# Performance work log

Hardware: AMD Instinct MI355X
Metric: run time of the kernel (lower is better)

## Reference

```python
import jax, jax.numpy as jnp
import numpy as np

B, IN, ED, PW, OUT, CL, NK = 2048, 4096, 8192, 2048, 256, 16, 32
MIX = 0.5

def _onehot_mask(key, n):
    # near-one-hot selector matrix [n, NK], as built by forward_update_masks
    idx = jax.random.choice(key, n, (NK,), replace=False)
    return jnp.zeros((n, NK), jnp.float32).at[idx, jnp.arange(NK)].set(1.0)

def setup_inputs():
    ks = jax.random.split(jax.random.key(0), 24)
    f = jnp.float32
    adj = (jax.random.uniform(ks[4], (IN, IN)) < 0.01).astype(f)
    adj = jnp.maximum(adj, adj.T).at[jnp.arange(IN), jnp.arange(IN)].set(1.0)
    return {
        'x_gene': jax.random.normal(ks[0], (B, IN), f),
        'x_invmea': jax.random.normal(ks[1], (B, IN), f),
        'x_curv': jax.random.normal(ks[2], (B, ED), f),
        'clinn': jax.random.normal(ks[3], (B, CL), f),
        'Adj': adj,
        'edge_mask': (jax.random.uniform(ks[5], (ED, IN)) < 0.005).astype(f),
        'pathway_mask': (jax.random.uniform(ks[6], (PW, ED)) < 0.02).astype(f),
        'top_gene_mask': _onehot_mask(ks[7], IN),
        'top_invmea_mask': _onehot_mask(ks[8], IN),
        'top_curv_mask': _onehot_mask(ks[9], ED),
        'top_path_mask': _onehot_mask(ks[10], PW),
        'W1': jnp.full((IN, IN), 0.05, f),
        'b1': 0.01 * jax.random.normal(ks[11], (IN,), f),
        'W2': jnp.full((ED, IN), 0.05, f),
        'b2': 0.01 * jax.random.normal(ks[12], (ED,), f),
        'W3': jnp.full((PW, ED), 0.05, f),
        'b3': 0.01 * jax.random.normal(ks[13], (PW,), f),
        'W4': 0.02 * jax.random.normal(ks[14], (OUT, PW), f),
        'b4': 0.01 * jax.random.normal(ks[15], (OUT,), f),
        'W5': 0.02 * jax.random.normal(ks[16], (OUT, OUT), f),
        'b5': 0.01 * jax.random.normal(ks[17], (OUT,), f),
        'W6': 0.05 * jax.random.normal(ks[18], (OUT, OUT + CL + 4 * NK), f),
        'W7': 0.05 * jax.random.normal(ks[19], (1, OUT), f),
        'mp11': MIX * jnp.ones(IN, f),
        'mp12': (1.0 - MIX) * jnp.ones(IN, f),
        'mp1': jnp.ones(IN, f),
        'mp21': MIX * jnp.ones(ED, f),
        'mp22': (1.0 - MIX) * jnp.ones(ED, f),
        'mp2': jnp.ones(ED, f),
        'mp3': jnp.ones(PW, f),
    }

def reference(x_gene, x_invmea, x_curv, clinn, Adj, edge_mask, pathway_mask,
              top_gene_mask, top_invmea_mask, top_curv_mask, top_path_mask,
              W1, b1, W2, b2, W3, b3, W4, b4, W5, b5, W6, W7,
              mp11, mp12, mp1, mp21, mp22, mp2, mp3):
    sg = jax.lax.stop_gradient
    sig = jax.nn.sigmoid
    kept_gene = sg(x_gene @ top_gene_mask)                     # [B,NK] gather-as-matmul
    x1 = sig(x_gene @ (W1 * Adj).T + b1)                       # masked linear [B,IN]
    x1 = x_invmea * (mp11 * mp1) + x1 * (mp12 * mp1)
    kept_invmea = sg(x1 @ top_invmea_mask)
    x1 = sig(x1 @ (W2 * edge_mask).T + b2)                     # [B,ED]
    x1 = x_curv * (mp21 * mp2) + x1 * (mp22 * mp2)
    kept_curv = sg(x1 @ top_curv_mask)
    x1 = sig(x1 @ (W3 * pathway_mask).T + b3)                  # [B,PW]
    x1 = x1 * mp3
    kept_path = sg(x1 @ top_path_mask)
    x1 = sig(x1 @ W4.T + b4)
    x1 = sig(x1 @ W5.T + b5)                                   # [B,OUT]
    x_cat = jnp.concatenate([x1, kept_gene, kept_invmea, kept_curv, kept_path, clinn], axis=1)
    lp = sig(x_cat @ W6.T)
    lp = lp - jnp.mean(lp, axis=1, keepdims=True)
    return lp @ W7.T                                           # [B,1]
```

## Files before the change

### kernel.cpp

```cpp
#include <hip/hip_runtime.h>

typedef unsigned short u16;
typedef __attribute__((ext_vector_type(4))) float f32x4;
typedef __attribute__((ext_vector_type(8))) short s16x8;

__device__ __forceinline__ u16 f2bf(float f) {
    union { float f; unsigned u; } c; c.f = f;
    return (u16)((c.u + 0x7fffu + ((c.u >> 16) & 1u)) >> 16);
}
__device__ __forceinline__ float bf2f(u16 u) {
    union { unsigned u; float f; } c; c.u = ((unsigned)u) << 16; return c.f;
}
__device__ __forceinline__ unsigned pk2(float a, float b) {
    return (unsigned)f2bf(a) | ((unsigned)f2bf(b) << 16);
}
__device__ __forceinline__ float sigm(float x) { return 1.0f / (1.0f + __expf(-x)); }
__device__ __forceinline__ void fma2(unsigned xv, float w, float& a0, float& a1) {
    union { float f; unsigned u; } lo, hi;
    lo.u = xv << 16; hi.u = xv & 0xFFFF0000u;
    a0 += w * lo.f; a1 += w * hi.f;
}

__device__ __forceinline__ void load16_g2l(const void* g, void* l) {
    __builtin_amdgcn_global_load_lds(
        (const __attribute__((address_space(1))) unsigned int*)(unsigned long long)g,
        (__attribute__((address_space(3))) unsigned int*)(unsigned int)(unsigned long long)l,
        16, 0, 0);
}

__device__ void d_transpF(const float* __restrict__ in, u16* __restrict__ out,
                          int Rr, int Cc, int bx, int by, float (*t)[65]) {
    const int r0 = by * 64, c0 = bx * 64;
    const int tid = threadIdx.x;
#pragma unroll
    for (int i = 0; i < 16; i++) {
        int idx = tid + i * 256;
        int rr = idx >> 6, cc = idx & 63;
        t[rr][cc] = in[(size_t)(r0 + rr) * Cc + c0 + cc];
    }
    __syncthreads();
#pragma unroll
    for (int i = 0; i < 16; i++) {
        int idx = tid + i * 256;
        int cc = idx >> 6, rr = idx & 63;
        out[(size_t)(c0 + cc) * Rr + r0 + rr] = f2bf(t[rr][cc]);
    }
}

__device__ void d_ell(const float* __restrict__ M, const float* __restrict__ W,
                      unsigned* __restrict__ ell, int* __restrict__ cnt,
                      int C, int PAD, int R, int bid) {
    const int lane = threadIdx.x & 63;
    const int row = bid * 4 + (threadIdx.x >> 6);
    if (row >= R) return;
    const float* mrow = M + (size_t)row * C;
    const float* wrow = W + (size_t)row * C;
    int n = 0;
    for (int c = lane * 4; c < C; c += 256) {
        float4 m = *(const float4*)(mrow + c);
        n += (m.x != 0.f) + (m.y != 0.f) + (m.z != 0.f) + (m.w != 0.f);
    }
    int pre = n;
#pragma unroll
    for (int off = 1; off < 64; off <<= 1) {
        int t = __shfl_up(pre, off, 64);
        if (lane >= off) pre += t;
    }
    int s = pre - n;
    unsigned* erow = ell + (size_t)row * PAD;
    for (int c = lane * 4; c < C; c += 256) {
        float4 m = *(const float4*)(mrow + c);
        if (m.x != 0.f) { if (s < PAD) erow[s] = ((unsigned)f2bf(wrow[c + 0]) << 16) | (unsigned)(c + 0); s++; }
        if (m.y != 0.f) { if (s < PAD) erow[s] = ((unsigned)f2bf(wrow[c + 1]) << 16) | (unsigned)(c + 1); s++; }
        if (m.z != 0.f) { if (s < PAD) erow[s] = ((unsigned)f2bf(wrow[c + 2]) << 16) | (unsigned)(c + 2); s++; }
        if (m.w != 0.f) { if (s < PAD) erow[s] = ((unsigned)f2bf(wrow[c + 3]) << 16) | (unsigned)(c + 3); s++; }
    }
    int tot = __shfl(pre, 63, 64);
    if (lane == 0) cnt[row] = tot > PAD ? PAD : tot;
}

__device__ void d_find(const float* __restrict__ mask, int n, int* __restrict__ outp,
                       int* red) {
    int best = -1;
    for (int i = threadIdx.x; i < n; i += 256)
        if (mask[(size_t)i * 32 + (blockIdx.x & 31)] != 0.0f) best = i;
    red[threadIdx.x] = best;
    __syncthreads();
    for (int off = 128; off > 0; off >>= 1) {
        if (threadIdx.x < off) {
            int o = red[threadIdx.x + off];
            if (o > red[threadIdx.x]) red[threadIdx.x] = o;
        }
        __syncthreads();
    }
    if (threadIdx.x == 0) *outp = red[0] < 0 ? 0 : red[0];
}

__device__ void d_conv(const float* __restrict__ in, u16* __restrict__ out,
                       int bid, unsigned n8) {
    unsigned i = bid * 256u + threadIdx.x;
    if (i >= n8) return;
    float4 a = ((const float4*)in)[2 * i];
    float4 b = ((const float4*)in)[2 * i + 1];
    uint4 o;
    o.x = pk2(a.x, a.y); o.y = pk2(a.z, a.w);
    o.z = pk2(b.x, b.y); o.w = pk2(b.z, b.w);
    ((uint4*)out)[i] = o;
}

__global__ __launch_bounds__(256) void prep_all(
    const float* __restrict__ xg_f, const float* __restrict__ xinv_f,
    const float* __restrict__ xcv_f,
    u16* __restrict__ xTg, u16* __restrict__ xinvT, u16* __restrict__ xcvT,
    const float* __restrict__ Adj, const float* __restrict__ W1,
    unsigned* __restrict__ ell1, int* __restrict__ cnt1,
    const float* __restrict__ edge, const float* __restrict__ W2,
    unsigned* __restrict__ ell2, int* __restrict__ cnt2,
    const float* __restrict__ path, const float* __restrict__ W3,
    unsigned* __restrict__ ell3, int* __restrict__ cnt3,
    const float* __restrict__ m0, const float* __restrict__ m1,
    const float* __restrict__ m2, const float* __restrict__ m3,
    int* __restrict__ idx,
    const float* __restrict__ W4, u16* __restrict__ w4b,
    const float* __restrict__ W5, u16* __restrict__ w5b) {
    __shared__ float tile[64][65];
    int id = blockIdx.x;
    if (id < 2048) { d_transpF(xg_f, xTg, 2048, 4096, id & 63, id >> 6, tile); return; }
    id -= 2048;
    if (id < 2048) { d_transpF(xinv_f, xinvT, 2048, 4096, id & 63, id >> 6, tile); return; }
    id -= 2048;
    if (id < 4096) { d_transpF(xcv_f, xcvT, 2048, 8192, id & 127, id >> 7, tile); return; }
    id -= 4096;
    if (id < 1024) { d_ell(Adj, W1, ell1, cnt1, 4096, 256, 4096, id); return; }
    id -= 1024;
    if (id < 2048) { d_ell(edge, W2, ell2, cnt2, 4096, 96, 8192, id); return; }
    id -= 2048;
    if (id < 512) { d_ell(path, W3, ell3, cnt3, 8192, 320, 2048, id); return; }
    id -= 512;
    if (id < 128) {
        const float* mk; int n;
        int which = id >> 5;
        if (which == 0)      { mk = m0; n = 4096; }
        else if (which == 1) { mk = m1; n = 4096; }
        else if (which == 2) { mk = m2; n = 8192; }
        else                 { mk = m3; n = 2048; }
        d_find(mk, n, idx + which * 32 + (id & 31), (int*)tile);
        return;
    }
    id -= 128;
    if (id < 256) { d_conv(W4, w4b, id, 65536u); return; }
    id -= 256;
    d_conv(W5, w5b, id, 8192u);
}

template <int BPL>
__global__ __launch_bounds__(256) void spmm(const unsigned* __restrict__ ell,
                                            const int* __restrict__ cnt,
                                            const u16* __restrict__ xT,
                                            u16* __restrict__ outT,
                                            const float* __restrict__ bias,
                                            const float* __restrict__ c1a,
                                            const float* __restrict__ c1b,
                                            const float* __restrict__ c2a,
                                            const float* __restrict__ c2b,
                                            const u16* __restrict__ invT,
                                            int PAD) {
    const int lane = threadIdx.x & 63;
    const int wv = __builtin_amdgcn_readfirstlane((int)(threadIdx.x >> 6));
    const int j = blockIdx.y * 4 + wv;
    const int b0 = blockIdx.x * (64 * BPL) + lane * BPL;

    const unsigned* ep = ell + (size_t)j * PAD;
    int len = cnt[j];
    if (len > PAD) len = PAD;

    float acc[BPL];
#pragma unroll
    for (int i = 0; i < BPL; i++) acc[i] = 0.f;

    const int nfull = len >> 3;
    unsigned eA[8];
    if (nfull > 0) {
#pragma unroll
        for (int t = 0; t < 8; t++) eA[t] = ep[t];
    }
    for (int g = 0; g < nfull; g++) {
        unsigned eB[8];
        const bool more = (g + 1 < nfull);
        if (more) {
#pragma unroll
            for (int t = 0; t < 8; t++) eB[t] = ep[(g + 1) * 8 + t];
        }
        if (BPL == 8) {
            uint4 xv[8];
#pragma unroll
            for (int t = 0; t < 8; t++)
                xv[t] = *(const uint4*)(xT + ((size_t)(eA[t] & 0xFFFFu) << 11) + b0);
#pragma unroll
            for (int t = 0; t < 8; t++) {
                union { float f; unsigned u; } w; w.u = (eA[t] >> 16) << 16;
                fma2(xv[t].x, w.f, acc[0], acc[1]);
                fma2(xv[t].y, w.f, acc[2], acc[3]);
                fma2(xv[t].z, w.f, acc[4], acc[5]);
                fma2(xv[t].w, w.f, acc[6], acc[7]);
            }
        } else {
            uint2 xv[8];
#pragma unroll
            for (int t = 0; t < 8; t++)
                xv[t] = *(const uint2*)(xT + ((size_t)(eA[t] & 0xFFFFu) << 11) + b0);
#pragma unroll
            for (int t = 0; t < 8; t++) {
                union { float f; unsigned u; } w; w.u = (eA[t] >> 16) << 16;
                fma2(xv[t].x, w.f, acc[0], acc[1]);
                fma2(xv[t].y, w.f, acc[2], acc[3]);
            }
        }
        if (more) {
#pragma unroll
            for (int t = 0; t < 8; t++) eA[t] = eB[t];
        }
    }
    for (int s = nfull * 8; s < len; ++s) {
        unsigned e = ep[s];
        union { float f; unsigned u; } w; w.u = (e >> 16) << 16;
        const u16* xp = xT + ((size_t)(e & 0xFFFFu) << 11) + b0;
        if (BPL == 8) {
            uint4 xv = *(const uint4*)xp;
            fma2(xv.x, w.f, acc[0], acc[1]); fma2(xv.y, w.f, acc[2], acc[3]);
            fma2(xv.z, w.f, acc[4], acc[5]); fma2(xv.w, w.f, acc[6], acc[7]);
        } else {
            uint2 xv = *(const uint2*)xp;
            fma2(xv.x, w.f, acc[0], acc[1]); fma2(xv.y, w.f, acc[2], acc[3]);
        }
    }

    const float bi = bias[j];
    float c1 = 0.f;
    if (c1a) { c1 = c1a[j]; if (c1b) c1 *= c1b[j]; }
    float c2 = 1.f;
    if (c2a) { c2 = c2a[j]; if (c2b) c2 *= c2b[j]; }

    float v[BPL];
#pragma unroll
    for (int i = 0; i < BPL; i++) v[i] = sigm(acc[i] + bi) * c2;
    if (invT) {
        const unsigned long long* ip = (const unsigned long long*)(invT + ((size_t)j << 11) + b0);
#pragma unroll
        for (int h = 0; h < BPL / 4; h++) {
            unsigned long long iv = __builtin_nontemporal_load(ip + h);
            unsigned lo = (unsigned)iv, hi = (unsigned)(iv >> 32);
            union { float f; unsigned u; } g0, g1, g2, g3;
            g0.u = lo << 16; g1.u = lo & 0xFFFF0000u;
            g2.u = hi << 16; g3.u = hi & 0xFFFF0000u;
            v[4 * h + 0] += g0.f * c1; v[4 * h + 1] += g1.f * c1;
            v[4 * h + 2] += g2.f * c1; v[4 * h + 3] += g3.f * c1;
        }
    }
    unsigned long long* op = (unsigned long long*)(outT + ((size_t)j << 11) + b0);
#pragma unroll
    for (int h = 0; h < BPL / 4; h++) {
        unsigned long long ov = (unsigned long long)pk2(v[4 * h + 0], v[4 * h + 1])
                              | ((unsigned long long)pk2(v[4 * h + 2], v[4 * h + 3]) << 32);
        __builtin_nontemporal_store(ov, op + h);
    }
}

__global__ __launch_bounds__(256) void gatherFT(const float* __restrict__ src, int ld,
                                                const int* __restrict__ idx,
                                                u16* __restrict__ dstT) {
    int i = blockIdx.x * 256 + threadIdx.x;
    int kk = i >> 11, b = i & 2047;
    dstT[i] = f2bf(src[(size_t)b * ld + idx[kk]]);
}
__global__ __launch_bounds__(256) void gatherT(const u16* __restrict__ xT,
                                               const int* __restrict__ idx,
                                               u16* __restrict__ dstT) {
    int i = blockIdx.x * 256 + threadIdx.x;
    int kk = i >> 11, b = i & 2047;
    dstT[i] = xT[(size_t)idx[kk] * 2048 + b];
}

__global__ __launch_bounds__(256) void transpB(const u16* __restrict__ in,
                                               u16* __restrict__ out, int Rr, int Cc) {
    __shared__ u16 t[64][66];
    const int r0 = blockIdx.y * 64, c0 = blockIdx.x * 64;
    const int tid = threadIdx.x;
#pragma unroll
    for (int i = 0; i < 16; i++) {
        int idx = tid + i * 256;
        int rr = idx >> 6, cc = idx & 63;
        t[rr][cc] = in[(size_t)(r0 + rr) * Cc + c0 + cc];
    }
    __syncthreads();
#pragma unroll
    for (int i = 0; i < 16; i++) {
        int idx = tid + i * 256;
        int cc = idx >> 6, rr = idx & 63;
        out[(size_t)(c0 + cc) * Rr + r0 + rr] = t[rr][cc];
    }
}

template <int WR, int WC, int MF, int NF, int KC, int WPE>
__global__ __launch_bounds__(WR * WC * 64, WPE)
void gemm_t(const u16* __restrict__ A, const u16* __restrict__ W,
            u16* __restrict__ Out, const float* __restrict__ bias, int N, int K) {
    constexpr int NTHR = WR * WC * 64;
    constexpr int BM = WR * MF * 16;
    constexpr int BN = WC * NF * 16;
    constexpr int BK = KC * 32;
    constexpr int CPR = KC * 4;
    constexpr int MSK = CPR - 1;
    constexpr int CA = BM * CPR / NTHR;
    constexpr int CB = BN * CPR / NTHR;
    constexpr int L  = CA + CB;

    __shared__ u16 At[2][BM * BK];
    __shared__ u16 Bt[2][BN * BK];

    const int tid = threadIdx.x;
    const int lane = tid & 63;
    const int wave = tid >> 6;
    const int wr = wave / WC, wc = wave % WC;
    const int tn = blockIdx.x, tm = blockIdx.y;
    const int r16 = lane & 15;
    const int q = lane >> 4;

    const u16* aSrc[CA]; int aDst[CA];
#pragma unroll
    for (int j = 0; j < CA; j++) {
        int c = tid + j * NTHR;
        int r = c / CPR, p = c - r * CPR;
        aSrc[j] = A + (size_t)(tm * BM + r) * K + (p ^ (r & MSK)) * 8;
        aDst[j] = c * 8;
    }
    const u16* bSrc[CB]; int bDst[CB];
#pragma unroll
    for (int j = 0; j < CB; j++) {
        int c = tid + j * NTHR;
        int r = c / CPR, p = c - r * CPR;
        bSrc[j] = W + (size_t)(tn * BN + r) * K + (p ^ (r & MSK)) * 8;
        bDst[j] = c * 8;
    }
    int aRd[MF][KC], bRd[NF][KC];
#pragma unroll
    for (int mi = 0; mi < MF; mi++)
#pragma unroll
        for (int kc = 0; kc < KC; kc++)
            aRd[mi][kc] = (wr * MF * 16 + mi * 16 + r16) * BK + (((kc * 4 + q) ^ (r16 & MSK)) << 3);
#pragma unroll
    for (int ni = 0; ni < NF; ni++)
#pragma unroll
        for (int kc = 0; kc < KC; kc++)
            bRd[ni][kc] = (wc * NF * 16 + ni * 16 + r16) * BK + (((kc * 4 + q) ^ (r16 & MSK)) << 3);

    const int nIter = K / BK;

#define ISSUE(slot, it_)                                              \
    do {                                                              \
        const int k0_ = (it_) * BK;                                   \
        _Pragma("unroll")                                             \
        for (int j = 0; j < CA; j++)                                  \
            load16_g2l(aSrc[j] + k0_, &At[slot][aDst[j]]);            \
        _Pragma("unroll")                                             \
        for (int j = 0; j < CB; j++)                                  \
            load16_g2l(bSrc[j] + k0_, &Bt[slot][bDst[j]]);            \
    } while (0)

    ISSUE(0, 0);
    if (nIter > 1) ISSUE(1, 1);

    f32x4 acc[MF][NF];
#pragma unroll
    for (int i = 0; i < MF; i++)
#pragma unroll
        for (int j = 0; j < NF; j++) acc[i][j] = (f32x4){0.f, 0.f, 0.f, 0.f};

    for (int it = 0; it < nIter; ++it) {
        const int s = it & 1;
        if (it + 1 < nIter) __builtin_amdgcn_s_waitcnt(0xF70 | L);
        else                __builtin_amdgcn_s_waitcnt(0xF70);
        __asm__ volatile("" ::: "memory");
        __builtin_amdgcn_s_barrier();
        __asm__ volatile("" ::: "memory");

        s16x8 af[KC][MF], bfr[KC][NF];
#pragma unroll
        for (int kc = 0; kc < KC; kc++) {
#pragma unroll
            for (int mi = 0; mi < MF; mi++) af[kc][mi] = *(const s16x8*)(&At[s][aRd[mi][kc]]);
#pragma unroll
            for (int ni = 0; ni < NF; ni++) bfr[kc][ni] = *(const s16x8*)(&Bt[s][bRd[ni][kc]]);
        }
        __asm__ volatile("" ::: "memory");
        __builtin_amdgcn_s_waitcnt(0xC07F);
        __builtin_amdgcn_s_barrier();
        __asm__ volatile("" ::: "memory");

        if (it + 2 < nIter) ISSUE(s, it + 2);

#pragma unroll
        for (int kc = 0; kc < KC; kc++)
#pragma unroll
            for (int mi = 0; mi < MF; mi++)
#pragma unroll
                for (int ni = 0; ni < NF; ni++)
                    acc[mi][ni] = __builtin_amdgcn_mfma_f32_16x16x32_bf16(af[kc][mi], bfr[kc][ni], acc[mi][ni], 0, 0, 0);
    }
#undef ISSUE

#pragma unroll
    for (int ni = 0; ni < NF; ni++) {
        const int n = tn * BN + wc * NF * 16 + ni * 16 + r16;
        const float bi = bias ? bias[n] : 0.f;
#pragma unroll
        for (int mi = 0; mi < MF; mi++) {
#pragma unroll
            for (int rg = 0; rg < 4; rg++) {
                const int m = tm * BM + wr * MF * 16 + mi * 16 + q * 4 + rg;
                Out[(size_t)m * N + n] = f2bf(sigm(acc[mi][ni][rg] + bi));
            }
        }
    }
}

__global__ __launch_bounds__(256) void tail_k(const u16* __restrict__ x5,
                                              const u16* __restrict__ kgT,
                                              const u16* __restrict__ kiT,
                                              const u16* __restrict__ kcT,
                                              const u16* __restrict__ kpT,
                                              const float* __restrict__ clinn,
                                              const float* __restrict__ W6,
                                              const float* __restrict__ W7,
                                              float* __restrict__ out) {
    __shared__ float xs[8 * 400];
    __shared__ float s1[4][8], s2[4][8], s3[4];
    const int tid = threadIdx.x;
    const int b0 = blockIdx.x * 8;
    for (int i = tid; i < 8 * 400; i += 256) {
        int r = i / 400, c = i - r * 400;
        int b = b0 + r;
        float v;
        if (c < 256)      v = bf2f(x5[b * 256 + c]);
        else if (c < 288) v = bf2f(kgT[(c - 256) * 2048 + b]);
        else if (c < 320) v = bf2f(kiT[(c - 288) * 2048 + b]);
        else if (c < 352) v = bf2f(kcT[(c - 320) * 2048 + b]);
        else if (c < 384) v = bf2f(kpT[(c - 352) * 2048 + b]);
        else              v = clinn[b * 16 + (c - 384)];
        xs[i] = v;
    }
    __syncthreads();
    const int j = tid;
    float acc[8];
#pragma unroll
    for (int r = 0; r < 8; r++) acc[r] = 0.f;
    const float4* wrow = (const float4*)(W6 + (size_t)j * 400);
    for (int c = 0; c < 100; c++) {
        float4 wv = wrow[c];
        const float* wp = (const float*)&wv;
#pragma unroll
        for (int t = 0; t < 4; t++) {
            float w = wp[t];
            int k = c * 4 + t;
#pragma unroll
            for (int r = 0; r < 8; r++) acc[r] += w * xs[r * 400 + k];
        }
    }
    const float w7j = W7[j];
    const int lane = tid & 63, wave = tid >> 6;
    float t3 = w7j;
#pragma unroll
    for (int off = 32; off > 0; off >>= 1) t3 += __shfl_down(t3, off, 64);
    if (lane == 0) s3[wave] = t3;
#pragma unroll
    for (int r = 0; r < 8; r++) {
        float lp = sigm(acc[r]);
        float t1 = lp, t2 = lp * w7j;
#pragma unroll
        for (int off = 32; off > 0; off >>= 1) {
            t1 += __shfl_down(t1, off, 64);
            t2 += __shfl_down(t2, off, 64);
        }
        if (lane == 0) { s1[wave][r] = t1; s2[wave][r] = t2; }
    }
    __syncthreads();
    if (tid < 8) {
        float S1 = s1[0][tid] + s1[1][tid] + s1[2][tid] + s1[3][tid];
        float S2 = s2[0][tid] + s2[1][tid] + s2[2][tid] + s2[3][tid];
        float SW = s3[0] + s3[1] + s3[2] + s3[3];
        out[b0 + tid] = S2 - (S1 * (1.f / 256.f)) * SW;
    }
}

extern "C" void kernel_launch(void* const* d_in, const int* in_sizes, int n_in,
                              void* d_out, int out_size, void* d_ws, size_t ws_size,
                              hipStream_t stream) {
    const float* x_gene   = (const float*)d_in[0];
    const float* x_invmea = (const float*)d_in[1];
    const float* x_curv   = (const float*)d_in[2];
    const float* clinn    = (const float*)d_in[3];
    const float* Adj      = (const float*)d_in[4];
    const float* edge_m   = (const float*)d_in[5];
    const float* path_m   = (const float*)d_in[6];
    const float* tg_mask  = (const float*)d_in[7];
    const float* ti_mask  = (const float*)d_in[8];
    const float* tc_mask  = (const float*)d_in[9];
    const float* tp_mask  = (const float*)d_in[10];
    const float* W1 = (const float*)d_in[11];  const float* b1 = (const float*)d_in[12];
    const float* W2 = (const float*)d_in[13];  const float* b2 = (const float*)d_in[14];
    const float* W3 = (const float*)d_in[15];  const float* b3 = (const float*)d_in[16];
    const float* W4 = (const float*)d_in[17];  const float* b4 = (const float*)d_in[18];
    const float* W5 = (const float*)d_in[19];  const float* b5 = (const float*)d_in[20];
    const float* W6 = (const float*)d_in[21];
    const float* W7 = (const float*)d_in[22];
    const float* mp11 = (const float*)d_in[23];
    const float* mp12 = (const float*)d_in[24];
    const float* mp1  = (const float*)d_in[25];
    const float* mp21 = (const float*)d_in[26];
    const float* mp22 = (const float*)d_in[27];
    const float* mp2  = (const float*)d_in[28];
    const float* mp3  = (const float*)d_in[29];

    char* ws = (char*)d_ws;
    const float* nulf = nullptr;
    float* out = (float*)d_out;

    u16*  xTg   = (u16*)(ws + 0);
    u16*  xinvT = (u16*)(ws + 16777216);
    u16*  xcvT  = (u16*)(ws + 33554432);
    u16*  x1T   = (u16*)(ws + 67108864);
    u16*  x2T   = (u16*)(ws + 83886080);
    u16*  x3T   = (u16*)(ws + 117440512);
    u16*  x3    = (u16*)(ws + 125829120);
    unsigned* ell1 = (unsigned*)(ws + 134217728);
    unsigned* ell2 = (unsigned*)(ws + 138412032);
    unsigned* ell3 = (unsigned*)(ws + 141557760);
    int* cnt1 = (int*)(ws + 144179200);
    int* cnt2 = (int*)(ws + 144195584);
    int* cnt3 = (int*)(ws + 144228352);
    int* idxg = (int*)(ws + 144236544);
    int* idxi = idxg + 32;
    int* idxc = idxg + 64;
    int* idxp = idxg + 96;
    u16* kgT  = (u16*)(ws + 144237056);
    u16* kiT  = (u16*)(ws + 144368128);
    u16* kcT  = (u16*)(ws + 144499200);
    u16* kpT  = (u16*)(ws + 144630272);
    u16* w4b  = (u16*)(ws + 144761344);
    u16* w5b  = (u16*)(ws + 145809920);
    u16* x4   = (u16*)(ws + 145940992);
    u16* x5   = (u16*)(ws + 146989568);

    prep_all<<<12192, 256, 0, stream>>>(
        x_gene, x_invmea, x_curv, xTg, xinvT, xcvT,
        Adj, W1, ell1, cnt1, edge_m, W2, ell2, cnt2, path_m, W3, ell3, cnt3,
        tg_mask, ti_mask, tc_mask, tp_mask, idxg, W4, w4b, W5, w5b);
    gatherFT<<<256, 256, 0, stream>>>(x_gene, 4096, idxg, kgT);

    spmm<4><<<dim3(8, 1024), 256, 0, stream>>>(ell1, cnt1, xTg, x1T, b1,
                                               mp11, mp1, mp12, mp1, xinvT, 256);
    gatherT<<<256, 256, 0, stream>>>(x1T, idxi, kiT);

    spmm<4><<<dim3(8, 2048), 256, 0, stream>>>(ell2, cnt2, x1T, x2T, b2,
                                               mp21, mp2, mp22, mp2, xcvT, 96);
    gatherT<<<256, 256, 0, stream>>>(x2T, idxc, kcT);

    spmm<4><<<dim3(8, 512), 256, 0, stream>>>(ell3, cnt3, x2T, x3T, b3,
                                              nulf, nulf, mp3, nulf, (const u16*)nullptr, 320);
    gatherT<<<256, 256, 0, stream>>>(x3T, idxp, kpT);
    transpB<<<dim3(32, 32), 256, 0, stream>>>(x3T, x3, 2048, 2048);

    gemm_t<2, 2, 2, 2, 2, 4><<<dim3(4, 32), 256, 0, stream>>>(x3, w4b, x4, b4, 256, 2048);
    gemm_t<2, 2, 2, 2, 2, 4><<<dim3(4, 32), 256, 0, stream>>>(x4, w5b, x5, b5, 256, 256);

    tail_k<<<256, 256, 0, stream>>>(x5, kgT, kiT, kcT, kpT, clinn, W6, W7, out);
}
```

Baseline: 940.8 us.

## Split ELL build into register-buffered kernel and fuse top-k gathers into spmm epilogue

The ELL construction moves into its own kernel. Each wave now loads a row's mask once into registers as 16 float4 values per half, where before it read the mask twice, once to count and once to emit. The three gatherT launches are removed: each spmm block checks whether its output row is one of the 32 selected indices and writes the packed bf16 values straight into the kept buffer. This saves three launches and a reread of the mask, at the cost of a 32-iteration index scan per wave in the spmm epilogue and higher register use in the ELL builder.

```diff
diff --git a/kernel.cpp b/kernel.cpp
--- a/kernel.cpp
+++ b/kernel.cpp
@@ -47,43 +47,11 @@
     }
 }
 
-__device__ void d_ell(const float* __restrict__ M, const float* __restrict__ W,
-                      unsigned* __restrict__ ell, int* __restrict__ cnt,
-                      int C, int PAD, int R, int bid) {
-    const int lane = threadIdx.x & 63;
-    const int row = bid * 4 + (threadIdx.x >> 6);
-    if (row >= R) return;
-    const float* mrow = M + (size_t)row * C;
-    const float* wrow = W + (size_t)row * C;
-    int n = 0;
-    for (int c = lane * 4; c < C; c += 256) {
-        float4 m = *(const float4*)(mrow + c);
-        n += (m.x != 0.f) + (m.y != 0.f) + (m.z != 0.f) + (m.w != 0.f);
-    }
-    int pre = n;
-#pragma unroll
-    for (int off = 1; off < 64; off <<= 1) {
-        int t = __shfl_up(pre, off, 64);
-        if (lane >= off) pre += t;
-    }
-    int s = pre - n;
-    unsigned* erow = ell + (size_t)row * PAD;
-    for (int c = lane * 4; c < C; c += 256) {
-        float4 m = *(const float4*)(mrow + c);
-        if (m.x != 0.f) { if (s < PAD) erow[s] = ((unsigned)f2bf(wrow[c + 0]) << 16) | (unsigned)(c + 0); s++; }
-        if (m.y != 0.f) { if (s < PAD) erow[s] = ((unsigned)f2bf(wrow[c + 1]) << 16) | (unsigned)(c + 1); s++; }
-        if (m.z != 0.f) { if (s < PAD) erow[s] = ((unsigned)f2bf(wrow[c + 2]) << 16) | (unsigned)(c + 2); s++; }
-        if (m.w != 0.f) { if (s < PAD) erow[s] = ((unsigned)f2bf(wrow[c + 3]) << 16) | (unsigned)(c + 3); s++; }
-    }
-    int tot = __shfl(pre, 63, 64);
-    if (lane == 0) cnt[row] = tot > PAD ? PAD : tot;
-}
-
 __device__ void d_find(const float* __restrict__ mask, int n, int* __restrict__ outp,
-                       int* red) {
+                       int* red, int k) {
     int best = -1;
     for (int i = threadIdx.x; i < n; i += 256)
-        if (mask[(size_t)i * 32 + (blockIdx.x & 31)] != 0.0f) best = i;
+        if (mask[(size_t)i * 32 + k] != 0.0f) best = i;
     red[threadIdx.x] = best;
     __syncthreads();
     for (int off = 128; off > 0; off >>= 1) {
@@ -108,16 +76,10 @@
     ((uint4*)out)[i] = o;
 }
 
-__global__ __launch_bounds__(256) void prep_all(
+__global__ __launch_bounds__(256) void prep_misc(
     const float* __restrict__ xg_f, const float* __restrict__ xinv_f,
     const float* __restrict__ xcv_f,
     u16* __restrict__ xTg, u16* __restrict__ xinvT, u16* __restrict__ xcvT,
-    const float* __restrict__ Adj, const float* __restrict__ W1,
-    unsigned* __restrict__ ell1, int* __restrict__ cnt1,
-    const float* __restrict__ edge, const float* __restrict__ W2,
-    unsigned* __restrict__ ell2, int* __restrict__ cnt2,
-    const float* __restrict__ path, const float* __restrict__ W3,
-    unsigned* __restrict__ ell3, int* __restrict__ cnt3,
     const float* __restrict__ m0, const float* __restrict__ m1,
     const float* __restrict__ m2, const float* __restrict__ m3,
     int* __restrict__ idx,
@@ -131,12 +93,6 @@
     id -= 2048;
     if (id < 4096) { d_transpF(xcv_f, xcvT, 2048, 8192, id & 127, id >> 7, tile); return; }
     id -= 4096;
-    if (id < 1024) { d_ell(Adj, W1, ell1, cnt1, 4096, 256, 4096, id); return; }
-    id -= 1024;
-    if (id < 2048) { d_ell(edge, W2, ell2, cnt2, 4096, 96, 8192, id); return; }
-    id -= 2048;
-    if (id < 512) { d_ell(path, W3, ell3, cnt3, 8192, 320, 2048, id); return; }
-    id -= 512;
     if (id < 128) {
         const float* mk; int n;
         int which = id >> 5;
@@ -144,13 +100,68 @@
         else if (which == 1) { mk = m1; n = 4096; }
         else if (which == 2) { mk = m2; n = 8192; }
         else                 { mk = m3; n = 2048; }
-        d_find(mk, n, idx + which * 32 + (id & 31), (int*)tile);
+        d_find(mk, n, idx + which * 32 + (id & 31), (int*)tile, id & 31);
         return;
     }
     id -= 128;
     if (id < 256) { d_conv(W4, w4b, id, 65536u); return; }
     id -= 256;
     d_conv(W5, w5b, id, 8192u);
+}
+
+template <int HALVES>
+__device__ void d_ell_reg(const float* __restrict__ M, const float* __restrict__ W,
+                          unsigned* __restrict__ ell, int* __restrict__ cnt,
+                          int PAD, int R, int bid) {
+    const int lane = threadIdx.x & 63;
+    const int row = bid * 4 + (threadIdx.x >> 6);
+    if (row >= R) return;
+    const float4* mrow = (const float4*)(M + (size_t)row * (HALVES * 4096));
+    const float* wrow = W + (size_t)row * (HALVES * 4096);
+    unsigned* erow = ell + (size_t)row * PAD;
+    int base = 0;
+#pragma unroll
+    for (int h = 0; h < HALVES; h++) {
+        float4 m[16];
+#pragma unroll
+        for (int i = 0; i < 16; i++) m[i] = mrow[h * 1024 + lane + i * 64];
+        int n = 0;
+#pragma unroll
+        for (int i = 0; i < 16; i++)
+            n += (m[i].x != 0.f) + (m[i].y != 0.f) + (m[i].z != 0.f) + (m[i].w != 0.f);
+        int pre = n;
+#pragma unroll
+        for (int off = 1; off < 64; off <<= 1) {
+            int t = __shfl_up(pre, off, 64);
+            if (lane >= off) pre += t;
+        }
+        int s = base + pre - n;
+#pragma unroll
+        for (int i = 0; i < 16; i++) {
+            int c = h * 4096 + lane * 4 + i * 256;
+            if (m[i].x != 0.f) { if (s < PAD) erow[s] = ((unsigned)f2bf(wrow[c + 0]) << 16) | (unsigned)(c + 0); s++; }
+            if (m[i].y != 0.f) { if (s < PAD) erow[s] = ((unsigned)f2bf(wrow[c + 1]) << 16) | (unsigned)(c + 1); s++; }
+            if (m[i].z != 0.f) { if (s < PAD) erow[s] = ((unsigned)f2bf(wrow[c + 2]) << 16) | (unsigned)(c + 2); s++; }
+            if (m[i].w != 0.f) { if (s < PAD) erow[s] = ((unsigned)f2bf(wrow[c + 3]) << 16) | (unsigned)(c + 3); s++; }
+        }
+        base += __shfl(pre, 63, 64);
+    }
+    if (lane == 0) cnt[row] = base > PAD ? PAD : base;
+}
+
+__global__ __launch_bounds__(256) void prep_ell(
+    const float* __restrict__ Adj, const float* __restrict__ W1,
+    unsigned* __restrict__ ell1, int* __restrict__ cnt1,
+    const float* __restrict__ edge, const float* __restrict__ W2,
+    unsigned* __restrict__ ell2, int* __restrict__ cnt2,
+    const float* __restrict__ path, const float* __restrict__ W3,
+    unsigned* __restrict__ ell3, int* __restrict__ cnt3) {
+    int id = blockIdx.x;
+    if (id < 1024) { d_ell_reg<1>(Adj, W1, ell1, cnt1, 256, 4096, id); return; }
+    id -= 1024;
+    if (id < 2048) { d_ell_reg<1>(edge, W2, ell2, cnt2, 96, 8192, id); return; }
+    id -= 2048;
+    d_ell_reg<2>(path, W3, ell3, cnt3, 320, 2048, id);
 }
 
 template <int BPL>
@@ -164,6 +175,8 @@
                                             const float* __restrict__ c2a,
                                             const float* __restrict__ c2b,
                                             const u16* __restrict__ invT,
+                                            const int* __restrict__ gidx,
+                                            u16* __restrict__ gdst,
                                             int PAD) {
     const int lane = threadIdx.x & 63;
     const int wv = __builtin_amdgcn_readfirstlane((int)(threadIdx.x >> 6));
@@ -257,12 +270,23 @@
             v[4 * h + 2] += g2.f * c1; v[4 * h + 3] += g3.f * c1;
         }
     }
+    unsigned long long pkv[BPL / 4];
+#pragma unroll
+    for (int h = 0; h < BPL / 4; h++)
+        pkv[h] = (unsigned long long)pk2(v[4 * h + 0], v[4 * h + 1])
+               | ((unsigned long long)pk2(v[4 * h + 2], v[4 * h + 3]) << 32);
     unsigned long long* op = (unsigned long long*)(outT + ((size_t)j << 11) + b0);
 #pragma unroll
-    for (int h = 0; h < BPL / 4; h++) {
-        unsigned long long ov = (unsigned long long)pk2(v[4 * h + 0], v[4 * h + 1])
-                              | ((unsigned long long)pk2(v[4 * h + 2], v[4 * h + 3]) << 32);
-        __builtin_nontemporal_store(ov, op + h);
+    for (int h = 0; h < BPL / 4; h++) __builtin_nontemporal_store(pkv[h], op + h);
+
+    if (gdst) {
+        for (int t = 0; t < 32; t++) {
+            if (gidx[t] == j) {
+                unsigned long long* gp = (unsigned long long*)(gdst + t * 2048 + b0);
+#pragma unroll
+                for (int h = 0; h < BPL / 4; h++) gp[h] = pkv[h];
+            }
+        }
     }
 }
 
@@ -272,13 +296,6 @@
     int i = blockIdx.x * 256 + threadIdx.x;
     int kk = i >> 11, b = i & 2047;
     dstT[i] = f2bf(src[(size_t)b * ld + idx[kk]]);
-}
-__global__ __launch_bounds__(256) void gatherT(const u16* __restrict__ xT,
-                                               const int* __restrict__ idx,
-                                               u16* __restrict__ dstT) {
-    int i = blockIdx.x * 256 + threadIdx.x;
-    int kk = i >> 11, b = i & 2047;
-    dstT[i] = xT[(size_t)idx[kk] * 2048 + b];
 }
 
 __global__ __launch_bounds__(256) void transpB(const u16* __restrict__ in,
@@ -551,23 +568,22 @@
     u16* x4   = (u16*)(ws + 145940992);
     u16* x5   = (u16*)(ws + 146989568);
 
-    prep_all<<<12192, 256, 0, stream>>>(
+    prep_ell<<<3584, 256, 0, stream>>>(
+        Adj, W1, ell1, cnt1, edge_m, W2, ell2, cnt2, path_m, W3, ell3, cnt3);
+    prep_misc<<<8608, 256, 0, stream>>>(
         x_gene, x_invmea, x_curv, xTg, xinvT, xcvT,
-        Adj, W1, ell1, cnt1, edge_m, W2, ell2, cnt2, path_m, W3, ell3, cnt3,
         tg_mask, ti_mask, tc_mask, tp_mask, idxg, W4, w4b, W5, w5b);
     gatherFT<<<256, 256, 0, stream>>>(x_gene, 4096, idxg, kgT);
 
     spmm<4><<<dim3(8, 1024), 256, 0, stream>>>(ell1, cnt1, xTg, x1T, b1,
-                                               mp11, mp1, mp12, mp1, xinvT, 256);
-    gatherT<<<256, 256, 0, stream>>>(x1T, idxi, kiT);
-
+                                               mp11, mp1, mp12, mp1, xinvT,
+                                               idxi, kiT, 256);
     spmm<4><<<dim3(8, 2048), 256, 0, stream>>>(ell2, cnt2, x1T, x2T, b2,
-                                               mp21, mp2, mp22, mp2, xcvT, 96);
-    gatherT<<<256, 256, 0, stream>>>(x2T, idxc, kcT);
-
+                                               mp21, mp2, mp22, mp2, xcvT,
+                                               idxc, kcT, 96);
     spmm<4><<<dim3(8, 512), 256, 0, stream>>>(ell3, cnt3, x2T, x3T, b3,
-                                              nulf, nulf, mp3, nulf, (const u16*)nullptr, 320);
-    gatherT<<<256, 256, 0, stream>>>(x3T, idxp, kpT);
+                                              nulf, nulf, mp3, nulf, (const u16*)nullptr,
+                                              idxp, kpT, 320);
     transpB<<<dim3(32, 32), 256, 0, stream>>>(x3T, x3, 2048, 2048);
 
     gemm_t<2, 2, 2, 2, 2, 4><<<dim3(4, 32), 256, 0, stream>>>(x3, w4b, x4, b4, 256, 2048);
```

Result: faster. 911.1 us (-3.2%).
